# Kernel optimization log

Hardware: AMD Instinct MI355X
Metric: run time of the kernel (lower is better)

Reference implementation:

```python
import jax, jax.numpy as jnp
import numpy as np

B, C, W, H = 8, 256, 64, 64
CQ = C // 8  # f/g projection dim


def setup_inputs() -> dict:
    key = jax.random.key(0)
    ks = jax.random.split(key, 8)
    x = jax.random.normal(ks[0], (B, C, W, H), dtype=jnp.float32)
    y = jax.random.normal(ks[1], (B, C, W, H), dtype=jnp.float32)
    # 1x1 conv weights stored as [out, in] matrices (xavier-uniform-like scale)
    def xavier(k, o, i):
        lim = float(np.sqrt(6.0 / (o + i)))
        return jax.random.uniform(k, (o, i), dtype=jnp.float32, minval=-lim, maxval=lim)
    Wf = xavier(ks[2], CQ, C); bf = jnp.zeros((CQ,), jnp.float32)
    Wg = xavier(ks[3], CQ, C); bg = jnp.zeros((CQ,), jnp.float32)
    Wh = xavier(ks[4], C, C);  bh = jnp.zeros((C,), jnp.float32)
    gamma = jnp.zeros((1,), jnp.float32)
    return {"x": x, "y": y, "Wf": Wf, "bf": bf, "Wg": Wg, "bg": bg,
            "Wh": Wh, "bh": bh, "gamma": gamma}


def reference(x, y, Wf, bf, Wg, bg, Wh, bh, gamma):
    b, c, w, h = x.shape
    n = w * h
    xf = x.reshape(b, c, n)  # [B,C,N]
    yf = y.reshape(b, c, n)
    f = jnp.einsum('dc,bcn->bdn', Wf, xf) + bf[None, :, None]  # [B,CQ,N]
    g = jnp.einsum('dc,bcn->bdn', Wg, yf) + bg[None, :, None]  # [B,CQ,N]
    hh = jnp.einsum('dc,bcn->bdn', Wh, xf) + bh[None, :, None]  # [B,C,N]
    # attention[b,i,j] = sum_d f[b,d,i] * g[b,d,j]; softmax over j (no 1/sqrt(d) scaling)
    attn = jax.nn.softmax(jnp.einsum('bdi,bdj->bij', f, g), axis=-1)  # [B,N,N]
    sa = jnp.einsum('bcn,bin->bci', hh, attn.transpose(0, 2, 1))  # h @ attn: [B,C,N]
    sa = jnp.einsum('bcj,bij->bci', hh, attn)  # equivalent, clean: sum_j h[:, :, j]*attn[:, i, j]
    out = gamma[0] * sa.reshape(b, c, w, h) + x
    return out
```

## Files before the change

### kernel.cpp

```cpp
#include <hip/hip_runtime.h>
#include <math.h>

#define BB      8
#define C_DIM   256
#define NN      4096
#define CQ_DIM  32
#define LOG2E   1.44269504088896f

typedef __bf16 bf16_t;
typedef bf16_t bf16x8 __attribute__((ext_vector_type(8)));
typedef float  f32x16 __attribute__((ext_vector_type(16)));

#if defined(__has_builtin)
#if __has_builtin(__builtin_amdgcn_exp2f)
#define EXP2F(x) __builtin_amdgcn_exp2f(x)
#else
#define EXP2F(x) exp2f(x)
#endif
#else
#define EXP2F(x) exp2f(x)
#endif

#define MFMA32(a, b, c) __builtin_amdgcn_mfma_f32_32x32x16_bf16((a), (b), (c), 0, 0, 0)

__device__ __forceinline__ void gload_lds16(const bf16_t* g, bf16_t* l)
{
    __builtin_amdgcn_global_load_lds(
        (const __attribute__((address_space(1))) void*)g,
        (__attribute__((address_space(3))) void*)l, 16, 0, 0);
}

__global__ __launch_bounds__(256) void cast_weights(
    const float* __restrict__ Wh, const float* __restrict__ Wf,
    const float* __restrict__ Wg, bf16_t* __restrict__ Whb,
    bf16_t* __restrict__ Wfb, bf16_t* __restrict__ Wgb)
{
    const int id = blockIdx.x * 256 + threadIdx.x;
    if (id < 65536)      Whb[id]         = (bf16_t)Wh[id];
    else if (id < 73728) Wfb[id - 65536] = (bf16_t)Wf[id - 65536];
    else if (id < 81920) Wgb[id - 73728] = (bf16_t)Wg[id - 73728];
}

__global__ __launch_bounds__(256) void transpose_cast(
    const float* __restrict__ src, bf16_t* __restrict__ dst)
{
    __shared__ float tile[64][65];
    const int b  = blockIdx.z;
    const int c0 = blockIdx.y * 64;
    const int n0 = blockIdx.x * 64;
    const int t  = threadIdx.x;
    const int col = t & 63, rbase = t >> 6;

#pragma unroll
    for (int rr = 0; rr < 16; ++rr) {
        const int crow = rbase + 4 * rr;
        tile[col][crow] = src[((size_t)b * C_DIM + c0 + crow) * NN + n0 + col];
    }
    __syncthreads();

    bf16_t* drow = dst + ((size_t)b * NN + n0) * C_DIM + c0;
#pragma unroll
    for (int p = 0; p < 2; ++p) {
        const int chunk = t + p * 256;
        const int nl = chunk >> 3, ck = chunk & 7;
        bf16x8 v;
#pragma unroll
        for (int j = 0; j < 8; ++j) v[j] = (bf16_t)tile[nl][ck * 8 + j];
        *(bf16x8*)(drow + (size_t)nl * C_DIM + ck * 8) = v;
    }
}

__global__ __launch_bounds__(128) void proj_qk_mfma(
    const bf16_t* __restrict__ Xt, const bf16_t* __restrict__ Wb,
    const float* __restrict__ bias, bf16_t* __restrict__ dst)
{
    const int id = blockIdx.x;
    const int b  = id & 7;
    const int n0 = (id >> 3) * 128;
    const int t  = threadIdx.x;
    const int w = t >> 6, lane = t & 63, l31 = lane & 31, half = lane >> 5;
    const int nbase = n0 + w * 64;

    const bf16_t* Ap = Wb + l31 * C_DIM + half * 8;
    const bf16_t* Bp = Xt + ((size_t)b * NN + nbase + l31) * C_DIM + half * 8;

    f32x16 acc[2] = {{}, {}};
    for (int c0 = 0; c0 < C_DIM; c0 += 16) {
        const bf16x8 af = *(const bf16x8*)(Ap + c0);
        const bf16x8 b0 = *(const bf16x8*)(Bp + c0);
        const bf16x8 b1 = *(const bf16x8*)(Bp + 32 * C_DIM + c0);
        acc[0] = MFMA32(af, b0, acc[0]);
        acc[1] = MFMA32(af, b1, acc[1]);
    }
#pragma unroll
    for (int nt = 0; nt < 2; ++nt)
#pragma unroll
        for (int r = 0; r < 16; ++r) {
            const int d = (r & 3) + 8 * (r >> 2) + 4 * half;
            const int n = nbase + nt * 32 + l31;
            dst[((size_t)b * NN + n) * CQ_DIM + d] = (bf16_t)(acc[nt][r] + bias[d]);
        }
}

__global__ __launch_bounds__(256) void proj_v_mfma(
    const bf16_t* __restrict__ Xt, const bf16_t* __restrict__ Wb,
    const float* __restrict__ bias, bf16_t* __restrict__ dst)
{
    const int id = blockIdx.x;
    const int b  = id & 7;
    const int r2 = id >> 3;
    const int m0 = (r2 & 3) * 64;
    const int n0 = (r2 >> 2) * 256;
    const int t  = threadIdx.x;
    const int w = t >> 6, lane = t & 63, l31 = lane & 31, half = lane >> 5;
    const int nbase = n0 + w * 64;

    const bf16_t* Ap = Wb + (m0 + l31) * C_DIM + half * 8;
    const bf16_t* Bp = Xt + ((size_t)b * NN + nbase + l31) * C_DIM + half * 8;

    f32x16 acc[2][2] = {{{}, {}}, {{}, {}}};
    for (int c0 = 0; c0 < C_DIM; c0 += 16) {
        const bf16x8 a0 = *(const bf16x8*)(Ap + c0);
        const bf16x8 a1 = *(const bf16x8*)(Ap + 32 * C_DIM + c0);
        const bf16x8 b0 = *(const bf16x8*)(Bp + c0);
        const bf16x8 b1 = *(const bf16x8*)(Bp + 32 * C_DIM + c0);
        acc[0][0] = MFMA32(a0, b0, acc[0][0]);
        acc[0][1] = MFMA32(a0, b1, acc[0][1]);
        acc[1][0] = MFMA32(a1, b0, acc[1][0]);
        acc[1][1] = MFMA32(a1, b1, acc[1][1]);
    }
#pragma unroll
    for (int mt = 0; mt < 2; ++mt)
#pragma unroll
        for (int nt = 0; nt < 2; ++nt)
#pragma unroll
            for (int r = 0; r < 16; ++r) {
                const int co = m0 + mt * 32 + (r & 3) + 8 * (r >> 2) + 4 * half;
                const int n  = nbase + nt * 32 + l31;
                dst[((size_t)b * C_DIM + co) * NN + n] = (bf16_t)(acc[mt][nt][r] + bias[co]);
            }
}

__global__ __launch_bounds__(512, 2) void attn_fused(
    const bf16_t* __restrict__ Q, const bf16_t* __restrict__ K,
    const bf16_t* __restrict__ V, const float* __restrict__ x,
    const float* __restrict__ gamma, float* __restrict__ out)
{
    const int id = blockIdx.x;
    const int b  = id & 7;
    const int i0 = (id >> 3) * 64;
    const int t  = threadIdx.x;
    const int w = t >> 6, lane = t & 63, l31 = lane & 31, half = lane >> 5;
    const int qg = w >> 2;
    const int jg = w & 3;
    const int cbx = ((jg & 1) << 2) | (jg & 2);

    __shared__ __align__(16) bf16_t Vlds[2][256 * 128];
    __shared__ float lpart[4 * 64];
    __shared__ float linv_s[64];

    const int r8h = 8 * half;

    const bf16_t* Qp = Q + ((size_t)(b * NN + i0 + qg * 32 + l31)) * CQ_DIM + r8h;
    const bf16x8 qf0 = *(const bf16x8*)Qp;
    const bf16x8 qf1 = *(const bf16x8*)(Qp + 16);

    const int pj = (l31 & 19) | ((l31 & 4) << 1) | ((l31 & 8) >> 1);
    const bf16_t* Kcur = K + ((size_t)b * NN + jg * 32 + pj) * CQ_DIM + r8h;

    const int sa = lane & 15, sb = lane >> 4;
    const bf16_t* Vrow0 = V + ((size_t)b * C_DIM + w * 32 + sb) * NN;
    int joff[8];
#pragma unroll
    for (int i = 0; i < 8; ++i)
        joff[i] = 8 * (sa ^ ((i * 4 + sb) & 15));

    const int vsw  = l31 & 15;
    const int vrow = l31 * 128;
    const int p0 = (((jg * 4) + half) ^ vsw) << 3;
    const int p1 = (((jg * 4) + 2 + half) ^ vsw) << 3;

    float lacc = 0.f;
    f32x16 O[8] = {{}, {}, {}, {}, {}, {}, {}, {}};
    bf16x8 frag[2];

    bf16_t* vcur = &Vlds[0][0];
    bf16_t* vnxt = &Vlds[1][0];

    auto do_stage = [&](int j0e, bf16_t* vb) {
        bf16_t* d = vb + w * 4096;
#pragma unroll
        for (int i = 0; i < 8; ++i)
            gload_lds16(Vrow0 + (size_t)(i * 4) * NN + j0e + joff[i],
                        d + i * 512);
    };

    auto do_S = [&]() {
        const bf16x8 kf0 = *(const bf16x8*)Kcur;
        const bf16x8 kf1 = *(const bf16x8*)(Kcur + 16);
        Kcur += 128 * CQ_DIM;
        f32x16 s = {};
        s = MFMA32(kf0, qf0, s);
        s = MFMA32(kf1, qf1, s);
        bf16x8 q0, q1;
#pragma unroll
        for (int r = 0; r < 8; ++r) {
            const float pv = EXP2F(s[r] * LOG2E);
            lacc += pv; q0[r] = (bf16_t)pv;
        }
#pragma unroll
        for (int r = 8; r < 16; ++r) {
            const float pv = EXP2F(s[r] * LOG2E);
            lacc += pv; q1[r - 8] = (bf16_t)pv;
        }
        frag[0] = q0;
        frag[1] = q1;
    };

    auto do_PV = [&](const bf16_t* vb) {
#pragma unroll
        for (int i = 0; i < 8; ++i) {
            const int rb = ((i ^ cbx) << 12) + vrow;
            const bf16x8 v0 = *(const bf16x8*)&vb[rb + p0];
            const bf16x8 v1 = *(const bf16x8*)&vb[rb + p1];
            O[i] = MFMA32(frag[0], v0, O[i]);
            O[i] = MFMA32(frag[1], v1, O[i]);
        }
    };

    do_stage(0, vcur);
    do_S();
    __syncthreads();

    for (int tt = 0; tt < 31; ++tt) {
        do_stage((tt + 1) * 128, vnxt);
        do_PV(vcur);
        do_S();
        __syncthreads();
        bf16_t* tmp = vcur; vcur = vnxt; vnxt = tmp;
    }
    do_PV(vcur);

    lacc += __shfl_xor(lacc, 32, 64);
    if (half == 0) lpart[jg * 64 + qg * 32 + l31] = lacc;
    __syncthreads();
    if (t < 64)
        linv_s[t] = 1.0f / (lpart[t] + lpart[64 + t] + lpart[128 + t] + lpart[192 + t]);

    float* red = (float*)&Vlds[0][0];
    const int qsw  = l31 & 7;
    const int myA  = w * 4096;

    {
        float* s = red + myA;
#pragma unroll
        for (int k = 0; k < 4; ++k)
#pragma unroll
            for (int r4 = 0; r4 < 4; ++r4) {
                const int quad = 2 * r4 + half;
                float4 v4 = { O[4 + k][4 * r4 + 0], O[4 + k][4 * r4 + 1],
                              O[4 + k][4 * r4 + 2], O[4 + k][4 * r4 + 3] };
                *(float4*)&s[k * 1024 + l31 * 32 + ((quad ^ qsw) << 2)] = v4;
            }
    }
    __syncthreads();
    {
        const float* s = red + (w ^ 1) * 4096;
#pragma unroll
        for (int k = 0; k < 4; ++k)
#pragma unroll
            for (int r4 = 0; r4 < 4; ++r4) {
                const int quad = 2 * r4 + half;
                const float4 v4 = *(const float4*)&s[k * 1024 + l31 * 32 + ((quad ^ qsw) << 2)];
                O[k][4 * r4 + 0] += v4.x;
                O[k][4 * r4 + 1] += v4.y;
                O[k][4 * r4 + 2] += v4.z;
                O[k][4 * r4 + 3] += v4.w;
            }
    }
    __syncthreads();
    {
        float* s = red + myA;
#pragma unroll
        for (int k = 0; k < 2; ++k)
#pragma unroll
            for (int r4 = 0; r4 < 4; ++r4) {
                const int quad = 2 * r4 + half;
                float4 v4 = { O[2 + k][4 * r4 + 0], O[2 + k][4 * r4 + 1],
                              O[2 + k][4 * r4 + 2], O[2 + k][4 * r4 + 3] };
                *(float4*)&s[k * 1024 + l31 * 32 + ((quad ^ qsw) << 2)] = v4;
            }
    }
    __syncthreads();
    {
        const float* s = red + (w ^ 2) * 4096;
#pragma unroll
        for (int k = 0; k < 2; ++k)
#pragma unroll
            for (int r4 = 0; r4 < 4; ++r4) {
                const int quad = 2 * r4 + half;
                const float4 v4 = *(const float4*)&s[k * 1024 + l31 * 32 + ((quad ^ qsw) << 2)];
                O[k][4 * r4 + 0] += v4.x;
                O[k][4 * r4 + 1] += v4.y;
                O[k][4 * r4 + 2] += v4.z;
                O[k][4 * r4 + 3] += v4.w;
            }
    }

    const float g = gamma[0];
#pragma unroll
    for (int k = 0; k < 2; ++k) {
        const int ch = (k ^ cbx) * 32 + l31;
        const size_t base = ((size_t)b * C_DIM + ch) * NN + i0 + qg * 32 + 4 * half;
#pragma unroll
        for (int r4 = 0; r4 < 4; ++r4) {
            const size_t idx = base + 8 * r4;
            const int rb = qg * 32 + 8 * r4 + 4 * half;
            const float4 xv = *(const float4*)(x + idx);
            float4 o;
            o.x = fmaf(g, O[k][4 * r4 + 0] * linv_s[rb + 0], xv.x);
            o.y = fmaf(g, O[k][4 * r4 + 1] * linv_s[rb + 1], xv.y);
            o.z = fmaf(g, O[k][4 * r4 + 2] * linv_s[rb + 2], xv.z);
            o.w = fmaf(g, O[k][4 * r4 + 3] * linv_s[rb + 3], xv.w);
            *(float4*)(out + idx) = o;
        }
    }
}

extern "C" void kernel_launch(void* const* d_in, const int* in_sizes, int n_in,
                              void* d_out, int out_size, void* d_ws, size_t ws_size,
                              hipStream_t stream)
{
    const float* x     = (const float*)d_in[0];
    const float* y     = (const float*)d_in[1];
    const float* Wf    = (const float*)d_in[2];
    const float* bf    = (const float*)d_in[3];
    const float* Wg    = (const float*)d_in[4];
    const float* bg    = (const float*)d_in[5];
    const float* Wh    = (const float*)d_in[6];
    const float* bh    = (const float*)d_in[7];
    const float* gamma = (const float*)d_in[8];
    float* out = (float*)d_out;

    bf16_t* bufA = (bf16_t*)d_ws;
    bf16_t* bufB = bufA + (size_t)BB * NN * C_DIM;
    bf16_t* Qw   = bufB + (size_t)BB * NN * C_DIM;
    bf16_t* Kw   = Qw + (size_t)BB * NN * CQ_DIM;
    bf16_t* Whb  = Kw + (size_t)BB * NN * CQ_DIM;
    bf16_t* Wfb  = Whb + C_DIM * C_DIM;
    bf16_t* Wgb  = Wfb + CQ_DIM * C_DIM;

    cast_weights<<<320, 256, 0, stream>>>(Wh, Wf, Wg, Whb, Wfb, Wgb);

    transpose_cast<<<dim3(NN / 64, C_DIM / 64, BB), 256, 0, stream>>>(y, bufA);
    proj_qk_mfma<<<BB * (NN / 128), 128, 0, stream>>>(bufA, Wgb, bg, Kw);

    transpose_cast<<<dim3(NN / 64, C_DIM / 64, BB), 256, 0, stream>>>(x, bufB);
    proj_qk_mfma<<<BB * (NN / 128), 128, 0, stream>>>(bufB, Wfb, bf, Qw);
    proj_v_mfma<<<BB * (C_DIM / 64) * (NN / 256), 256, 0, stream>>>(bufB, Whb, bh, bufA);

    attn_fused<<<BB * (NN / 64), 512, 0, stream>>>(Qw, Kw, bufA, x, gamma, out);
}
```

Before: 253.8 us.

## Fuse transpose-cast and Q/K/V projections into one prep kernel; prefetch K earlier

Replaces the two transpose_cast launches and three projection launches with a single prep_fused kernel. Each block transposes and casts a 64-position slab of x or y into swizzled LDS and computes Q/K (and V for x) directly from LDS, so the bf16 transposed intermediates never go to global memory. The attention loop also issues K-fragment loads before staging V, to hide their latency. The fused kernel uses a large LDS footprint and leaves half its waves idle during the Q/K projection, which may reduce occupancy and parallelism.

```diff
diff --git a/kernel.cpp b/kernel.cpp
--- a/kernel.cpp
+++ b/kernel.cpp
@@ -8,6 +8,7 @@
 #define LOG2E   1.44269504088896f
 
 typedef __bf16 bf16_t;
+typedef bf16_t bf16x4 __attribute__((ext_vector_type(4)));
 typedef bf16_t bf16x8 __attribute__((ext_vector_type(8)));
 typedef float  f32x16 __attribute__((ext_vector_type(16)));
 
@@ -41,104 +42,97 @@
     else if (id < 81920) Wgb[id - 73728] = (bf16_t)Wg[id - 73728];
 }
 
-__global__ __launch_bounds__(256) void transpose_cast(
-    const float* __restrict__ src, bf16_t* __restrict__ dst)
-{
-    __shared__ float tile[64][65];
-    const int b  = blockIdx.z;
-    const int c0 = blockIdx.y * 64;
-    const int n0 = blockIdx.x * 64;
-    const int t  = threadIdx.x;
+__global__ __launch_bounds__(256) void prep_fused(
+    const float* __restrict__ x, const float* __restrict__ y,
+    const bf16_t* __restrict__ Whb, const bf16_t* __restrict__ Wfb,
+    const bf16_t* __restrict__ Wgb,
+    const float* __restrict__ bh, const float* __restrict__ bfv,
+    const float* __restrict__ bg,
+    bf16_t* __restrict__ Qw, bf16_t* __restrict__ Kw, bf16_t* __restrict__ Vw)
+{
+    const int id   = blockIdx.x;
+    const bool isx = id < 512;
+    const int bid  = id & 511;
+    const int b    = bid & 7;
+    const int n0   = (bid >> 3) * 64;
+    const float* src = isx ? x : y;
+
+    __shared__ float ftile[64][65];
+    __shared__ __align__(16) bf16_t Xb[64 * 256];
+
+    const int t = threadIdx.x;
+    const int w = t >> 6, lane = t & 63, l31 = lane & 31, half = lane >> 5;
     const int col = t & 63, rbase = t >> 6;
 
-#pragma unroll
-    for (int rr = 0; rr < 16; ++rr) {
-        const int crow = rbase + 4 * rr;
-        tile[col][crow] = src[((size_t)b * C_DIM + c0 + crow) * NN + n0 + col];
-    }
-    __syncthreads();
-
-    bf16_t* drow = dst + ((size_t)b * NN + n0) * C_DIM + c0;
-#pragma unroll
-    for (int p = 0; p < 2; ++p) {
-        const int chunk = t + p * 256;
-        const int nl = chunk >> 3, ck = chunk & 7;
-        bf16x8 v;
-#pragma unroll
-        for (int j = 0; j < 8; ++j) v[j] = (bf16_t)tile[nl][ck * 8 + j];
-        *(bf16x8*)(drow + (size_t)nl * C_DIM + ck * 8) = v;
-    }
-}
-
-__global__ __launch_bounds__(128) void proj_qk_mfma(
-    const bf16_t* __restrict__ Xt, const bf16_t* __restrict__ Wb,
-    const float* __restrict__ bias, bf16_t* __restrict__ dst)
-{
-    const int id = blockIdx.x;
-    const int b  = id & 7;
-    const int n0 = (id >> 3) * 128;
-    const int t  = threadIdx.x;
-    const int w = t >> 6, lane = t & 63, l31 = lane & 31, half = lane >> 5;
-    const int nbase = n0 + w * 64;
-
-    const bf16_t* Ap = Wb + l31 * C_DIM + half * 8;
-    const bf16_t* Bp = Xt + ((size_t)b * NN + nbase + l31) * C_DIM + half * 8;
-
-    f32x16 acc[2] = {{}, {}};
-    for (int c0 = 0; c0 < C_DIM; c0 += 16) {
-        const bf16x8 af = *(const bf16x8*)(Ap + c0);
-        const bf16x8 b0 = *(const bf16x8*)(Bp + c0);
-        const bf16x8 b1 = *(const bf16x8*)(Bp + 32 * C_DIM + c0);
-        acc[0] = MFMA32(af, b0, acc[0]);
-        acc[1] = MFMA32(af, b1, acc[1]);
-    }
-#pragma unroll
-    for (int nt = 0; nt < 2; ++nt)
-#pragma unroll
-        for (int r = 0; r < 16; ++r) {
-            const int d = (r & 3) + 8 * (r >> 2) + 4 * half;
-            const int n = nbase + nt * 32 + l31;
-            dst[((size_t)b * NN + n) * CQ_DIM + d] = (bf16_t)(acc[nt][r] + bias[d]);
-        }
-}
-
-__global__ __launch_bounds__(256) void proj_v_mfma(
-    const bf16_t* __restrict__ Xt, const bf16_t* __restrict__ Wb,
-    const float* __restrict__ bias, bf16_t* __restrict__ dst)
-{
-    const int id = blockIdx.x;
-    const int b  = id & 7;
-    const int r2 = id >> 3;
-    const int m0 = (r2 & 3) * 64;
-    const int n0 = (r2 >> 2) * 256;
-    const int t  = threadIdx.x;
-    const int w = t >> 6, lane = t & 63, l31 = lane & 31, half = lane >> 5;
-    const int nbase = n0 + w * 64;
-
-    const bf16_t* Ap = Wb + (m0 + l31) * C_DIM + half * 8;
-    const bf16_t* Bp = Xt + ((size_t)b * NN + nbase + l31) * C_DIM + half * 8;
-
-    f32x16 acc[2][2] = {{{}, {}}, {{}, {}}};
-    for (int c0 = 0; c0 < C_DIM; c0 += 16) {
-        const bf16x8 a0 = *(const bf16x8*)(Ap + c0);
-        const bf16x8 a1 = *(const bf16x8*)(Ap + 32 * C_DIM + c0);
-        const bf16x8 b0 = *(const bf16x8*)(Bp + c0);
-        const bf16x8 b1 = *(const bf16x8*)(Bp + 32 * C_DIM + c0);
-        acc[0][0] = MFMA32(a0, b0, acc[0][0]);
-        acc[0][1] = MFMA32(a0, b1, acc[0][1]);
-        acc[1][0] = MFMA32(a1, b0, acc[1][0]);
-        acc[1][1] = MFMA32(a1, b1, acc[1][1]);
-    }
-#pragma unroll
-    for (int mt = 0; mt < 2; ++mt)
-#pragma unroll
-        for (int nt = 0; nt < 2; ++nt)
+    for (int cs = 0; cs < 4; ++cs) {
+        if (cs) __syncthreads();
+#pragma unroll
+        for (int rr = 0; rr < 16; ++rr) {
+            const int crow = rbase + 4 * rr;
+            ftile[col][crow] =
+                src[((size_t)b * C_DIM + cs * 64 + crow) * NN + n0 + col];
+        }
+        __syncthreads();
+#pragma unroll
+        for (int p = 0; p < 2; ++p) {
+            const int chunk = t + p * 256;
+            const int nl = chunk >> 3, ck = chunk & 7;
+            bf16x8 v;
+#pragma unroll
+            for (int j = 0; j < 8; ++j) v[j] = (bf16_t)ftile[nl][ck * 8 + j];
+            const int slot = (cs * 8 + ck) ^ (nl & 15);
+            *(bf16x8*)&Xb[nl * 256 + slot * 8] = v;
+        }
+    }
+    __syncthreads();
+
+    auto xbfrag = [&](int nloc, int s) -> bf16x8 {
+        return *(const bf16x8*)&Xb[nloc * 256 +
+                                   (((s * 2 + half) ^ (nloc & 15)) << 3)];
+    };
+
+    if (w < 2) {
+        const int nloc = w * 32 + l31;
+        const bf16_t* Wp = (isx ? Wfb : Wgb) + l31 * C_DIM + half * 8;
+        const float*  bp = isx ? bfv : bg;
+        f32x16 acc = {};
+        for (int s = 0; s < 16; ++s) {
+            const bf16x8 af = *(const bf16x8*)(Wp + s * 16);
+            acc = MFMA32(af, xbfrag(nloc, s), acc);
+        }
+        bf16_t* dst = (isx ? Qw : Kw) + ((size_t)b * NN + n0 + nloc) * CQ_DIM;
+#pragma unroll
+        for (int rq = 0; rq < 4; ++rq) {
+            const int d0 = 8 * rq + 4 * half;
+            bf16x4 v4;
+#pragma unroll
+            for (int ri = 0; ri < 4; ++ri)
+                v4[ri] = (bf16_t)(acc[4 * rq + ri] + bp[d0 + ri]);
+            *(bf16x4*)(dst + d0) = v4;
+        }
+    }
+
+    if (isx) {
+#pragma unroll
+        for (int mi = 0; mi < 2; ++mi) {
+            const int m = 2 * w + mi;
+            const bf16_t* Ap = Whb + (size_t)(m * 32 + l31) * C_DIM + half * 8;
+            f32x16 a0 = {}, a1 = {};
+            for (int s = 0; s < 16; ++s) {
+                const bf16x8 af = *(const bf16x8*)(Ap + s * 16);
+                a0 = MFMA32(af, xbfrag(l31, s), a0);
+                a1 = MFMA32(af, xbfrag(32 + l31, s), a1);
+            }
 #pragma unroll
             for (int r = 0; r < 16; ++r) {
-                const int co = m0 + mt * 32 + (r & 3) + 8 * (r >> 2) + 4 * half;
-                const int n  = nbase + nt * 32 + l31;
-                dst[((size_t)b * C_DIM + co) * NN + n] = (bf16_t)(acc[mt][nt][r] + bias[co]);
-            }
+                const int co = m * 32 + (r & 3) + 8 * (r >> 2) + 4 * half;
+                const float bb = bh[co];
+                bf16_t* vp = Vw + ((size_t)b * C_DIM + co) * NN + n0 + l31;
+                vp[0]  = (bf16_t)(a0[r] + bb);
+                vp[32] = (bf16_t)(a1[r] + bb);
+            }
+        }
+    }
 }
 
 __global__ __launch_bounds__(512, 2) void attn_fused(
@@ -195,10 +189,7 @@
                         d + i * 512);
     };
 
-    auto do_S = [&]() {
-        const bf16x8 kf0 = *(const bf16x8*)Kcur;
-        const bf16x8 kf1 = *(const bf16x8*)(Kcur + 16);
-        Kcur += 128 * CQ_DIM;
+    auto do_S = [&](const bf16x8 kf0, const bf16x8 kf1) {
         f32x16 s = {};
         s = MFMA32(kf0, qf0, s);
         s = MFMA32(kf1, qf1, s);
@@ -228,14 +219,22 @@
         }
     };
 
-    do_stage(0, vcur);
-    do_S();
+    {
+        const bf16x8 k0 = *(const bf16x8*)Kcur;
+        const bf16x8 k1 = *(const bf16x8*)(Kcur + 16);
+        Kcur += 128 * CQ_DIM;
+        do_stage(0, vcur);
+        do_S(k0, k1);
+    }
     __syncthreads();
 
     for (int tt = 0; tt < 31; ++tt) {
+        const bf16x8 k0 = *(const bf16x8*)Kcur;
+        const bf16x8 k1 = *(const bf16x8*)(Kcur + 16);
+        Kcur += 128 * CQ_DIM;
         do_stage((tt + 1) * 128, vnxt);
         do_PV(vcur);
-        do_S();
+        do_S(k0, k1);
         __syncthreads();
         bf16_t* tmp = vcur; vcur = vnxt; vnxt = tmp;
     }
@@ -248,8 +247,8 @@
         linv_s[t] = 1.0f / (lpart[t] + lpart[64 + t] + lpart[128 + t] + lpart[192 + t]);
 
     float* red = (float*)&Vlds[0][0];
-    const int qsw  = l31 & 7;
-    const int myA  = w * 4096;
+    const int qsw = l31 & 7;
+    const int myA = w * 4096;
 
     {
         float* s = red + myA;
@@ -343,21 +342,14 @@
     float* out = (float*)d_out;
 
     bf16_t* bufA = (bf16_t*)d_ws;
-    bf16_t* bufB = bufA + (size_t)BB * NN * C_DIM;
-    bf16_t* Qw   = bufB + (size_t)BB * NN * C_DIM;
+    bf16_t* Qw   = bufA + (size_t)BB * NN * C_DIM;
     bf16_t* Kw   = Qw + (size_t)BB * NN * CQ_DIM;
     bf16_t* Whb  = Kw + (size_t)BB * NN * CQ_DIM;
     bf16_t* Wfb  = Whb + C_DIM * C_DIM;
     bf16_t* Wgb  = Wfb + CQ_DIM * C_DIM;
 
     cast_weights<<<320, 256, 0, stream>>>(Wh, Wf, Wg, Whb, Wfb, Wgb);
-
-    transpose_cast<<<dim3(NN / 64, C_DIM / 64, BB), 256, 0, stream>>>(y, bufA);
-    proj_qk_mfma<<<BB * (NN / 128), 128, 0, stream>>>(bufA, Wgb, bg, Kw);
-
-    transpose_cast<<<dim3(NN / 64, C_DIM / 64, BB), 256, 0, stream>>>(x, bufB);
-    proj_qk_mfma<<<BB * (NN / 128), 128, 0, stream>>>(bufB, Wfb, bf, Qw);
-    proj_v_mfma<<<BB * (C_DIM / 64) * (NN / 256), 256, 0, stream>>>(bufB, Whb, bh, bufA);
-
+    prep_fused<<<1024, 256, 0, stream>>>(x, y, Whb, Wfb, Wgb,
+                                         bh, bf, bg, Qw, Kw, bufA);
     attn_fused<<<BB * (NN / 64), 512, 0, stream>>>(Qw, Kw, bufA, x, gamma, out);
 }
```

New measurement: 234.7 us. -7.5%, faster.
